# Kernel optimization log

Measured on AMD Instinct MI355X. Metric: run time of the kernel, lower is better.

## Reference

```python
import jax, jax.numpy as jnp
import numpy as np

B, N, C, H = 2, 4096, 256, 4
DH = C // H  # 64
EPS = 1e-6
TEMPERATURE = 1.0


def setup_inputs() -> dict:
    key = jax.random.key(0)
    ks = jax.random.split(key, 12)
    s = 0.02
    return {
        "x": jax.random.normal(ks[0], (B, N, C), dtype=jnp.float32),
        "pos_embed": jax.random.normal(ks[1], (B, N, C), dtype=jnp.float32),
        # per-head Q/K/V linear weights stacked over heads (torch Linear(dim, dim_head))
        "Wq": jax.random.normal(ks[2], (H, C, DH), dtype=jnp.float32) * s,
        "bq": jax.random.normal(ks[3], (H, DH), dtype=jnp.float32) * s,
        "Wk": jax.random.normal(ks[4], (H, C, DH), dtype=jnp.float32) * s,
        "bk": jax.random.normal(ks[5], (H, DH), dtype=jnp.float32) * s,
        "Wv": jax.random.normal(ks[6], (H, C, DH), dtype=jnp.float32) * s,
        "bv": jax.random.normal(ks[7], (H, DH), dtype=jnp.float32) * s,
        "Wo": jax.random.normal(ks[8], (C, C), dtype=jnp.float32) * s,
        "bo": jax.random.normal(ks[9], (C,), dtype=jnp.float32) * s,
        "ln_g": jnp.ones((C,), dtype=jnp.float32),
        "ln_b": jnp.zeros((C,), dtype=jnp.float32),
    }


def reference(x, pos_embed, Wq, bq, Wk, bk, Wv, bv, Wo, bo, ln_g, ln_b):
    dk = TEMPERATURE * jnp.sqrt(jnp.float32(DH))
    # pre-norm: x + pos_embed -> dropout(p=0, identity) -> LayerNorm(eps=1e-6)
    h = x + pos_embed
    mu = jnp.mean(h, axis=-1, keepdims=True)
    var = jnp.mean(jnp.square(h - mu), axis=-1, keepdims=True)
    h = (h - mu) * jax.lax.rsqrt(var + EPS) * ln_g + ln_b  # [B,N,C]
    # all heads at once (original loops over heads with separate small Linears)
    q = jnp.einsum("bnc,hcd->bhnd", h, Wq) + bq[None, :, None, :]
    k = jnp.einsum("bnc,hcd->bhnd", h, Wk) + bk[None, :, None, :]
    v = jnp.einsum("bnc,hcd->bhnd", h, Wv) + bv[None, :, None, :]
    scores = jnp.einsum("bhid,bhjd->bhij", q, k) / dk  # [B,H,N,N]
    # NOTE: original uses F.softmax(dot_prod, dim=1) on [B,N,N] -> normalize over
    # the QUERY axis i, not the key axis j. Replicated faithfully here (axis=2).
    attn = jax.nn.softmax(scores, axis=2)
    o = jnp.einsum("bhij,bhjd->bhid", attn, v)  # [B,H,N,DH]
    o = jnp.transpose(o, (0, 2, 1, 3)).reshape(B, N, C)  # concat heads on channel
    return o @ Wo + bo
```

## Files before the change

kernel.cpp:

```cpp
#include <hip/hip_runtime.h>
#include <math.h>

#define B_ 2
#define N_ 4096
#define C_ 256
#define H_ 4
#define DH_ 64
#define EPS_ 1e-6f
#define SCALE_Q_ 0.18033688011112042f

typedef short bf16x8 __attribute__((ext_vector_type(8)));
typedef short bf16x4v __attribute__((ext_vector_type(4)));
typedef float f32x4 __attribute__((ext_vector_type(4)));
typedef int i32x4 __attribute__((ext_vector_type(4)));

#define MFMA32(a, b, c) __builtin_amdgcn_mfma_f32_16x16x32_bf16(a, b, c, 0, 0, 0)
#define FAST_EXP2(x) __builtin_amdgcn_exp2f(x)

typedef const unsigned int __attribute__((address_space(1)))* gptr_as1;
typedef unsigned int __attribute__((address_space(3)))* lptr_as3;
#define GLL16(gp, lp)                                                   \
  __builtin_amdgcn_global_load_lds(                                     \
      (gptr_as1)(unsigned long long)(const void*)(gp),                  \
      (lptr_as3)(unsigned int)(unsigned long long)(const void*)(lp),    \
      16, 0, 0)

__device__ __forceinline__ unsigned short f2bf(float x) {
  unsigned int u = __float_as_uint(x);
  return (unsigned short)((u + 0x7FFFu + ((u >> 16) & 1u)) >> 16);
}
__device__ __forceinline__ float bf2f(unsigned short u) {
  return __uint_as_float(((unsigned int)u) << 16);
}
__device__ __forceinline__ int pack2bf(float lo, float hi) {
  return (int)__builtin_amdgcn_perm(__float_as_uint(hi) + 0x8000u,
                                    __float_as_uint(lo) + 0x8000u, 0x07060302u);
}

__global__ __launch_bounds__(256) void ln_kernel(
    const float* __restrict__ x, const float* __restrict__ pos,
    const float* __restrict__ g, const float* __restrict__ beta,
    unsigned short* __restrict__ h16) {
  const int w = threadIdx.x >> 6, lane = threadIdx.x & 63;
  const int row = blockIdx.x * 4 + w;
  const float4 xv = *(const float4*)&x[row * C_ + lane * 4];
  const float4 pv = *(const float4*)&pos[row * C_ + lane * 4];
  float4 v = {xv.x + pv.x, xv.y + pv.y, xv.z + pv.z, xv.w + pv.w};
  float s = v.x + v.y + v.z + v.w;
  s += __shfl_xor(s, 1);  s += __shfl_xor(s, 2);  s += __shfl_xor(s, 4);
  s += __shfl_xor(s, 8);  s += __shfl_xor(s, 16); s += __shfl_xor(s, 32);
  const float mu = s * (1.0f / C_);
  float4 d = {v.x - mu, v.y - mu, v.z - mu, v.w - mu};
  float q = d.x * d.x + d.y * d.y + d.z * d.z + d.w * d.w;
  q += __shfl_xor(q, 1);  q += __shfl_xor(q, 2);  q += __shfl_xor(q, 4);
  q += __shfl_xor(q, 8);  q += __shfl_xor(q, 16); q += __shfl_xor(q, 32);
  const float rs = rsqrtf(q * (1.0f / C_) + EPS_);
  const float4 g4 = *(const float4*)&g[lane * 4];
  const float4 b4 = *(const float4*)&beta[lane * 4];
  bf16x4v o;
  o[0] = (short)f2bf(d.x * rs * g4.x + b4.x);
  o[1] = (short)f2bf(d.y * rs * g4.y + b4.y);
  o[2] = (short)f2bf(d.z * rs * g4.z + b4.z);
  o[3] = (short)f2bf(d.w * rs * g4.w + b4.w);
  *(bf16x4v*)&h16[row * C_ + lane * 4] = o;
}

__global__ __launch_bounds__(256) void wconv_kernel(
    const float* __restrict__ Wq, const float* __restrict__ Wk,
    const float* __restrict__ Wv, const float* __restrict__ Wo,
    unsigned short* __restrict__ W3T, unsigned short* __restrict__ WoT) {
  const int base = blockIdx.x * 2048;
#pragma unroll
  for (int p = 0; p < 8; p++) {
    const int idx = base + p * 256 + threadIdx.x;
    if (idx < 196608) {
      const int m = idx >> 14;
      const int rem = idx & 16383;
      const int c = rem >> 6, d = rem & 63;
      const int h = m / 3, kind = m - h * 3;
      const float* W = kind == 0 ? Wq : kind == 1 ? Wk : Wv;
      float v = W[h * 16384 + rem];
      if (kind == 0) v *= SCALE_Q_;
      W3T[(h * 192 + kind * 64 + d) * 256 + c] = f2bf(v);
    } else {
      const int widx = idx - 196608;
      const int k = widx >> 8, n = widx & 255;
      WoT[n * 256 + k] = f2bf(Wo[widx]);
    }
  }
}

__global__ __launch_bounds__(256) void qkv_kernel(
    const unsigned short* __restrict__ h16, const unsigned short* __restrict__ W3T,
    const float* __restrict__ bq, const float* __restrict__ bk,
    const float* __restrict__ bv,
    unsigned short* __restrict__ q16, unsigned short* __restrict__ k16,
    unsigned short* __restrict__ vT16) {
  const int rt = blockIdx.x;
  const int hh = blockIdx.y;
  const int t = threadIdx.x;
  const int w = t >> 6, lane = t & 63, c = lane & 15, quad = lane >> 4;
  __shared__ unsigned short Hs[64 * 64];
  __shared__ unsigned short Bs[192 * 64];
  const int row0 = rt * 64;

  f32x4 acc[12];
#pragma unroll
  for (int nt = 0; nt < 12; nt++) acc[nt] = (f32x4){0.f, 0.f, 0.f, 0.f};

  for (int kt = 0; kt < C_; kt += 64) {
    __syncthreads();
#pragma unroll
    for (int p = 0; p < 2; p++) {
      const int e = t + p * 256;
      const int row = e >> 3, ch = e & 7;
      *(bf16x8*)&Hs[row * 64 + ((ch ^ (row & 7)) * 8)] =
          *(const bf16x8*)&h16[(size_t)(row0 + row) * C_ + kt + ch * 8];
    }
#pragma unroll
    for (int p = 0; p < 6; p++) {
      const int e = t + p * 256;
      const int row = e >> 3, ch = e & 7;
      *(bf16x8*)&Bs[row * 64 + ((ch ^ (row & 7)) * 8)] =
          *(const bf16x8*)&W3T[(size_t)(hh * 192 + row) * C_ + kt + ch * 8];
    }
    __syncthreads();
#pragma unroll
    for (int kh = 0; kh < 2; kh++) {
      const int i = w * 16 + c;
      bf16x8 a = *(const bf16x8*)&Hs[i * 64 + (((kh * 4 + quad) ^ (i & 7)) * 8)];
#pragma unroll
      for (int nt = 0; nt < 12; nt++) {
        const int n = nt * 16 + c;
        bf16x8 b = *(const bf16x8*)&Bs[n * 64 + (((kh * 4 + quad) ^ (n & 7)) * 8)];
        acc[nt] = MFMA32(a, b, acc[nt]);
      }
    }
  }
#pragma unroll
  for (int nt = 0; nt < 12; nt++) {
    const int kind = nt >> 2;
    const int col = (nt & 3) * 16 + c;
    const float bias = kind == 0 ? bq[hh * 64 + col] * SCALE_Q_
                     : kind == 1 ? bk[hh * 64 + col] : bv[hh * 64 + col];
#pragma unroll
    for (int r = 0; r < 4; r++) {
      const int gr = row0 + w * 16 + quad * 4 + r;
      const int b = gr >> 12, n = gr & (N_ - 1);
      const size_t bh = (size_t)(b * H_ + hh);
      const unsigned short val = f2bf(acc[nt][r] + bias);
      if (kind == 0)      q16[(bh * N_ + n) * DH_ + col] = val;
      else if (kind == 1) k16[(bh * N_ + n) * DH_ + col] = val;
      else                vT16[(bh * DH_ + col) * N_ + n] = val;
    }
  }
}

__global__ __launch_bounds__(256, 2) void colstats_kernel(
    const unsigned short* __restrict__ q16, const unsigned short* __restrict__ k16,
    unsigned short* __restrict__ vT16) {
  const int blk = blockIdx.x;
  const int bh = blk & 7;
  const int j0 = (blk >> 3) * 64;
  const int t = threadIdx.x;
  const int w = t >> 6, lane = t & 63, c = lane & 15, quad = lane >> 4;
  __shared__ __align__(16) unsigned short Qb[2 * 8192];
  __shared__ float Lp[4][64];
  __shared__ float ilv[64];

  bf16x8 ka[4][2];
#pragma unroll
  for (int jb = 0; jb < 4; jb++) {
    const size_t kb = ((size_t)bh * N_ + j0 + jb * 16 + c) * DH_;
    ka[jb][0] = *(const bf16x8*)&k16[kb + quad * 8];
    ka[jb][1] = *(const bf16x8*)&k16[kb + 32 + quad * 8];
  }

  const int rl = lane >> 3, sl = lane & 7;
  const unsigned short* gQ =
      q16 + ((size_t)bh * N_ + w * 32 + rl) * DH_ + ((sl ^ rl) * 8);
  const int woff = w * 2048;

  f32x4 lsum[4];
#pragma unroll
  for (int jb = 0; jb < 4; jb++) lsum[jb] = (f32x4){0.f, 0.f, 0.f, 0.f};

#pragma unroll
  for (int s = 0; s < 4; s++)
    GLL16(gQ + s * (8 * DH_), Qb + woff + s * 512);
  gQ += 128 * DH_;

  for (int r2 = 0; r2 < 32; r2 += 2) {
#pragma unroll
    for (int hf = 0; hf < 2; hf++) {
      const int cur = hf, nxt = hf ^ 1;
#pragma unroll
      for (int s = 0; s < 4; s++)
        GLL16(gQ + s * (8 * DH_), Qb + nxt * 8192 + woff + s * 512);
      gQ += 128 * DH_;
      asm volatile("s_waitcnt vmcnt(4)" ::: "memory");
      const unsigned short* Qs = Qb + cur * 8192 + woff;
#pragma unroll
      for (int u = 0; u < 2; u++) {
        bf16x8 qf0 = *(const bf16x8*)&Qs[u * 1024 + c * 64 + ((quad ^ (c & 7)) * 8)];
        bf16x8 qf1 = *(const bf16x8*)&Qs[u * 1024 + c * 64 + (((4 + quad) ^ (c & 7)) * 8)];
#pragma unroll
        for (int jb = 0; jb < 4; jb++) {
          f32x4 s = {0.f, 0.f, 0.f, 0.f};
          s = MFMA32(ka[jb][0], qf0, s);
          s = MFMA32(ka[jb][1], qf1, s);
#pragma unroll
          for (int r = 0; r < 4; r++) lsum[jb][r] += FAST_EXP2(s[r]);
        }
      }
    }
  }
#pragma unroll
  for (int jb = 0; jb < 4; jb++) {
#pragma unroll
    for (int r = 0; r < 4; r++) {
      float s = lsum[jb][r];
      s += __shfl_xor(s, 1); s += __shfl_xor(s, 2);
      s += __shfl_xor(s, 4); s += __shfl_xor(s, 8);
      if (c == 0) Lp[w][jb * 16 + quad * 4 + r] = s;
    }
  }
  __syncthreads();
  if (t < 64)
    ilv[t] = 1.0f / (Lp[0][t] + Lp[1][t] + Lp[2][t] + Lp[3][t]);
  __syncthreads();
  {
    const int d = t >> 2, chb = t & 3;
#pragma unroll
    for (int cc = 0; cc < 2; cc++) {
      const int ch = chb + cc * 4;
      const size_t addr = ((size_t)bh * DH_ + d) * N_ + j0 + ch * 8;
      bf16x8 v = *(const bf16x8*)&vT16[addr];
#pragma unroll
      for (int jj = 0; jj < 8; jj++)
        v[jj] = (short)f2bf(bf2f((unsigned short)v[jj]) * ilv[ch * 8 + jj]);
      *(bf16x8*)&vT16[addr] = v;
    }
  }
}

__global__ __launch_bounds__(512, 4) void attnout_kernel(
    const unsigned short* __restrict__ q16, const unsigned short* __restrict__ k16,
    const unsigned short* __restrict__ vT16, unsigned short* __restrict__ ob16) {
  const int blk = blockIdx.x;
  const int bh = blk & 7;
  const int bb = bh >> 2, hh = bh & 3;
  const int i0 = (blk >> 3) * 64;
  const int t = threadIdx.x;
  const int w = t >> 6, lane = t & 63, c = lane & 15, quad = lane >> 4;
  const int iw = w >> 2;
  const int jw = w & 3;

  __shared__ __align__(16) char smem[65536];
  unsigned short* S16 = (unsigned short*)smem;
  float* Rf = (float*)smem;

  bf16x8 qa[2][2];
#pragma unroll
  for (int ib = 0; ib < 2; ib++) {
    const size_t qb = ((size_t)bh * N_ + i0 + iw * 32 + ib * 16 + c) * DH_;
    qa[ib][0] = *(const bf16x8*)&q16[qb + quad * 8];
    qa[ib][1] = *(const bf16x8*)&q16[qb + 32 + quad * 8];
  }

  const int krow  = w * 16 + (lane >> 3);
  const int kch   = (lane & 7) ^ (((krow >> 2) & 7) ^ (krow & 3));
  const int krow2 = krow + 8;
  const int kch2  = (lane & 7) ^ (((krow2 >> 2) & 7) ^ (krow2 & 3));
  const unsigned short* gK  = k16 + ((size_t)bh * N_ + krow ) * DH_ + kch  * 8;
  const unsigned short* gK2 = k16 + ((size_t)bh * N_ + krow2) * DH_ + kch2 * 8;
  const int vd   = w * 8 + (lane >> 4);
  const int vch  = (lane & 15) ^ (vd & 15);
  const int vd2  = vd + 4;
  const int vch2 = (lane & 15) ^ (vd2 & 15);
  const unsigned short* gV  = vT16 + ((size_t)bh * DH_ + vd ) * N_ + vch  * 8;
  const unsigned short* gV2 = vT16 + ((size_t)bh * DH_ + vd2) * N_ + vch2 * 8;
  const int ldsKo = w * 1024;
  const int ldsVo = 8192 + w * 1024;

  f32x4 of[2][4];
#pragma unroll
  for (int ib = 0; ib < 2; ib++)
#pragma unroll
    for (int dt = 0; dt < 4; dt++) of[ib][dt] = (f32x4){0.f, 0.f, 0.f, 0.f};

  GLL16(gK,  S16 + ldsKo);       GLL16(gK2, S16 + ldsKo + 512);
  GLL16(gV,  S16 + ldsVo);       GLL16(gV2, S16 + ldsVo + 512);
  gK += 128 * DH_; gK2 += 128 * DH_; gV += 128; gV2 += 128;

  for (int jt = 0; jt < N_; jt += 256) {
#pragma unroll
    for (int half = 0; half < 2; half++) {
      const int cur = half, nxt = half ^ 1;
      GLL16(gK,  S16 + nxt * 16384 + ldsKo);
      GLL16(gK2, S16 + nxt * 16384 + ldsKo + 512);
      GLL16(gV,  S16 + nxt * 16384 + ldsVo);
      GLL16(gV2, S16 + nxt * 16384 + ldsVo + 512);
      gK += 128 * DH_; gK2 += 128 * DH_; gV += 128; gV2 += 128;
      asm volatile("s_waitcnt vmcnt(4)" ::: "memory");
      asm volatile("s_barrier" ::: "memory");
      const unsigned short* Ks = S16 + cur * 16384;
      const unsigned short* Vs = S16 + cur * 16384 + 8192;

      bf16x8 kf[2][2];
#pragma unroll
      for (int s = 0; s < 2; s++) {
        const int jr = jw * 32 + ((c >> 2) * 8) + s * 4 + (c & 3);
        const int swz = ((jr >> 2) & 7) ^ (jr & 3);
        kf[s][0] = *(const bf16x8*)&Ks[jr * 64 + ((quad ^ swz) * 8)];
        kf[s][1] = *(const bf16x8*)&Ks[jr * 64 + (((4 + quad) ^ swz) * 8)];
      }
      bf16x8 vf[4];
#pragma unroll
      for (int dt = 0; dt < 4; dt++) {
        const int d = dt * 16 + c;
        vf[dt] = *(const bf16x8*)&Vs[d * 128 + (((jw * 4 + quad) ^ (d & 15)) * 8)];
      }

      __builtin_amdgcn_s_setprio(1);
#pragma unroll
      for (int ib = 0; ib < 2; ib++) {
        f32x4 s0 = {0.f, 0.f, 0.f, 0.f}, s1 = {0.f, 0.f, 0.f, 0.f};
        s0 = MFMA32(kf[0][0], qa[ib][0], s0);
        s0 = MFMA32(kf[0][1], qa[ib][1], s0);
        s1 = MFMA32(kf[1][0], qa[ib][0], s1);
        s1 = MFMA32(kf[1][1], qa[ib][1], s1);
        i32x4 pi;
        pi[0] = pack2bf(FAST_EXP2(s0[0]), FAST_EXP2(s0[1]));
        pi[1] = pack2bf(FAST_EXP2(s0[2]), FAST_EXP2(s0[3]));
        pi[2] = pack2bf(FAST_EXP2(s1[0]), FAST_EXP2(s1[1]));
        pi[3] = pack2bf(FAST_EXP2(s1[2]), FAST_EXP2(s1[3]));
        bf16x8 pf = *(bf16x8*)&pi;
#pragma unroll
        for (int dt = 0; dt < 4; dt++)
          of[ib][dt] = MFMA32(pf, vf[dt], of[ib][dt]);
      }
      __builtin_amdgcn_s_setprio(0);
      asm volatile("s_barrier" ::: "memory");
    }
  }

  __syncthreads();
  if (jw >= 2) {
    float* dst = Rf + (iw * 2 + (jw - 2)) * 2048;
#pragma unroll
    for (int ib = 0; ib < 2; ib++)
#pragma unroll
      for (int dt = 0; dt < 4; dt++)
        *(f32x4*)&dst[lane * 32 + (((ib * 4 + dt) ^ (lane & 7)) * 4)] = of[ib][dt];
  }
  __syncthreads();
  if (jw < 2) {
    const float* src = Rf + (iw * 2 + jw) * 2048;
#pragma unroll
    for (int ib = 0; ib < 2; ib++)
#pragma unroll
      for (int dt = 0; dt < 4; dt++)
        of[ib][dt] += *(const f32x4*)&src[lane * 32 + (((ib * 4 + dt) ^ (lane & 7)) * 4)];
  }
  __syncthreads();
  if (jw == 1) {
    float* dst = Rf + iw * 2048;
#pragma unroll
    for (int ib = 0; ib < 2; ib++)
#pragma unroll
      for (int dt = 0; dt < 4; dt++)
        *(f32x4*)&dst[lane * 32 + (((ib * 4 + dt) ^ (lane & 7)) * 4)] = of[ib][dt];
  }
  __syncthreads();
  if (jw == 0) {
    const float* src = Rf + iw * 2048;
#pragma unroll
    for (int ib = 0; ib < 2; ib++)
#pragma unroll
      for (int dt = 0; dt < 4; dt++) {
        of[ib][dt] += *(const f32x4*)&src[lane * 32 + (((ib * 4 + dt) ^ (lane & 7)) * 4)];
#pragma unroll
        for (int r = 0; r < 4; r++)
          ob16[((size_t)bb * N_ + i0 + iw * 32 + ib * 16 + quad * 4 + r) * C_ +
               hh * DH_ + dt * 16 + c] = f2bf(of[ib][dt][r]);
      }
  }
}

__global__ __launch_bounds__(256) void outproj_kernel(
    const unsigned short* __restrict__ ob16, const unsigned short* __restrict__ WoT,
    const float* __restrict__ bo, float* __restrict__ out) {
  const int rt = blockIdx.x;
  const int ch2 = blockIdx.y;
  const int t = threadIdx.x;
  const int w = t >> 6, lane = t & 63, c = lane & 15, quad = lane >> 4;
  __shared__ unsigned short As[32 * 64];
  __shared__ unsigned short Bs[128 * 64];

  f32x4 acc[2][2];
#pragma unroll
  for (int mt = 0; mt < 2; mt++)
#pragma unroll
    for (int nt = 0; nt < 2; nt++) acc[mt][nt] = (f32x4){0.f, 0.f, 0.f, 0.f};

  for (int kt = 0; kt < C_; kt += 64) {
    __syncthreads();
    {
      const int row = t >> 3, ch = t & 7;
      *(bf16x8*)&As[row * 64 + ((ch ^ (row & 7)) * 8)] =
          *(const bf16x8*)&ob16[((size_t)rt * 32 + row) * C_ + kt + ch * 8];
    }
#pragma unroll
    for (int p = 0; p < 4; p++) {
      const int e = t + p * 256;
      const int row = e >> 3, ch = e & 7;
      *(bf16x8*)&Bs[row * 64 + ((ch ^ (row & 7)) * 8)] =
          *(const bf16x8*)&WoT[(size_t)(ch2 * 128 + row) * C_ + kt + ch * 8];
    }
    __syncthreads();
#pragma unroll
    for (int kh = 0; kh < 2; kh++) {
      bf16x8 a[2];
#pragma unroll
      for (int mt = 0; mt < 2; mt++) {
        const int i = mt * 16 + c;
        a[mt] = *(const bf16x8*)&As[i * 64 + (((kh * 4 + quad) ^ (i & 7)) * 8)];
      }
#pragma unroll
      for (int nt = 0; nt < 2; nt++) {
        const int n = w * 32 + nt * 16 + c;
        bf16x8 b = *(const bf16x8*)&Bs[n * 64 + (((kh * 4 + quad) ^ (n & 7)) * 8)];
        acc[0][nt] = MFMA32(a[0], b, acc[0][nt]);
        acc[1][nt] = MFMA32(a[1], b, acc[1][nt]);
      }
    }
  }
#pragma unroll
  for (int mt = 0; mt < 2; mt++)
#pragma unroll
    for (int nt = 0; nt < 2; nt++) {
      const int col = ch2 * 128 + w * 32 + nt * 16 + c;
      const float bias = bo[col];
#pragma unroll
      for (int r = 0; r < 4; r++)
        out[((size_t)rt * 32 + mt * 16 + quad * 4 + r) * C_ + col] = acc[mt][nt][r] + bias;
    }
}

extern "C" void kernel_launch(void* const* d_in, const int* in_sizes, int n_in,
                              void* d_out, int out_size, void* d_ws, size_t ws_size,
                              hipStream_t stream) {
  const float* x    = (const float*)d_in[0];
  const float* pos  = (const float*)d_in[1];
  const float* Wq   = (const float*)d_in[2];
  const float* bq   = (const float*)d_in[3];
  const float* Wk   = (const float*)d_in[4];
  const float* bk   = (const float*)d_in[5];
  const float* Wv   = (const float*)d_in[6];
  const float* bv   = (const float*)d_in[7];
  const float* Wo   = (const float*)d_in[8];
  const float* bo   = (const float*)d_in[9];
  const float* ln_g = (const float*)d_in[10];
  const float* ln_b = (const float*)d_in[11];
  float* out = (float*)d_out;

  const size_t SZ = (size_t)B_ * N_ * C_;
  unsigned short* h16  = (unsigned short*)d_ws;
  unsigned short* q16  = h16 + SZ;
  unsigned short* k16  = q16 + SZ;
  unsigned short* vT16 = k16 + SZ;
  unsigned short* ob16 = vT16 + SZ;
  unsigned short* W3T  = ob16 + SZ;
  unsigned short* WoT  = W3T + (size_t)H_ * 192 * 256;

  ln_kernel<<<B_ * N_ / 4, 256, 0, stream>>>(x, pos, ln_g, ln_b, h16);
  wconv_kernel<<<128, 256, 0, stream>>>(Wq, Wk, Wv, Wo, W3T, WoT);
  qkv_kernel<<<dim3(128, H_), 256, 0, stream>>>(h16, W3T, bq, bk, bv, q16, k16, vT16);
  colstats_kernel<<<512, 256, 0, stream>>>(q16, k16, vT16);
  attnout_kernel<<<512, 512, 0, stream>>>(q16, k16, vT16, ob16);
  outproj_kernel<<<dim3(256, 2), 256, 0, stream>>>(ob16, WoT, bo, out);
}
```

Measured before the change: 171.3 us.

## Halve attnout block to 4 waves, each covering all 64 query rows

Each attention-output block now runs 4 waves instead of 8. Every wave processes all 64 query rows (4 row-tiles) against its own slice of keys, where before two wave groups each took 32 rows. Each K/V fragment read from LDS now feeds twice as many MFMAs, and each wave issues more global-to-LDS loads. The cost is higher register pressure (more Q and accumulator fragments), fewer waves per block to hide latency, and a lower launch-bounds occupancy hint.

```diff
diff --git a/kernel.cpp b/kernel.cpp
--- a/kernel.cpp
+++ b/kernel.cpp
@@ -244,7 +244,7 @@
   }
 }
 
-__global__ __launch_bounds__(512, 4) void attnout_kernel(
+__global__ __launch_bounds__(256, 2) void attnout_kernel(
     const unsigned short* __restrict__ q16, const unsigned short* __restrict__ k16,
     const unsigned short* __restrict__ vT16, unsigned short* __restrict__ ob16) {
   const int blk = blockIdx.x;
@@ -253,56 +253,60 @@
   const int i0 = (blk >> 3) * 64;
   const int t = threadIdx.x;
   const int w = t >> 6, lane = t & 63, c = lane & 15, quad = lane >> 4;
-  const int iw = w >> 2;
-  const int jw = w & 3;
+  const int jw = w;
 
   __shared__ __align__(16) char smem[65536];
   unsigned short* S16 = (unsigned short*)smem;
   float* Rf = (float*)smem;
 
-  bf16x8 qa[2][2];
-#pragma unroll
-  for (int ib = 0; ib < 2; ib++) {
-    const size_t qb = ((size_t)bh * N_ + i0 + iw * 32 + ib * 16 + c) * DH_;
+  bf16x8 qa[4][2];
+#pragma unroll
+  for (int ib = 0; ib < 4; ib++) {
+    const size_t qb = ((size_t)bh * N_ + i0 + ib * 16 + c) * DH_;
     qa[ib][0] = *(const bf16x8*)&q16[qb + quad * 8];
     qa[ib][1] = *(const bf16x8*)&q16[qb + 32 + quad * 8];
   }
 
-  const int krow  = w * 16 + (lane >> 3);
-  const int kch   = (lane & 7) ^ (((krow >> 2) & 7) ^ (krow & 3));
-  const int krow2 = krow + 8;
-  const int kch2  = (lane & 7) ^ (((krow2 >> 2) & 7) ^ (krow2 & 3));
-  const unsigned short* gK  = k16 + ((size_t)bh * N_ + krow ) * DH_ + kch  * 8;
-  const unsigned short* gK2 = k16 + ((size_t)bh * N_ + krow2) * DH_ + kch2 * 8;
-  const int vd   = w * 8 + (lane >> 4);
-  const int vch  = (lane & 15) ^ (vd & 15);
-  const int vd2  = vd + 4;
-  const int vch2 = (lane & 15) ^ (vd2 & 15);
-  const unsigned short* gV  = vT16 + ((size_t)bh * DH_ + vd ) * N_ + vch  * 8;
-  const unsigned short* gV2 = vT16 + ((size_t)bh * DH_ + vd2) * N_ + vch2 * 8;
-  const int ldsKo = w * 1024;
-  const int ldsVo = 8192 + w * 1024;
-
-  f32x4 of[2][4];
-#pragma unroll
-  for (int ib = 0; ib < 2; ib++)
+  const int rl3 = lane >> 3, sl3 = lane & 7;
+  const int rl4 = lane >> 4, sl4 = lane & 15;
+  const unsigned short* gK[4];
+  const unsigned short* gV[4];
+#pragma unroll
+  for (int s = 0; s < 4; s++) {
+    const int kr = w * 32 + s * 8 + rl3;
+    const int kc = sl3 ^ (((kr >> 2) & 7) ^ (kr & 3));
+    gK[s] = k16 + ((size_t)bh * N_ + kr) * DH_ + kc * 8;
+    const int vd = w * 16 + s * 4 + rl4;
+    const int vc = sl4 ^ (vd & 15);
+    gV[s] = vT16 + ((size_t)bh * DH_ + vd) * N_ + vc * 8;
+  }
+  const int ldsKo = w * 2048;
+  const int ldsVo = 8192 + w * 2048;
+
+  f32x4 of[4][4];
+#pragma unroll
+  for (int ib = 0; ib < 4; ib++)
 #pragma unroll
     for (int dt = 0; dt < 4; dt++) of[ib][dt] = (f32x4){0.f, 0.f, 0.f, 0.f};
 
-  GLL16(gK,  S16 + ldsKo);       GLL16(gK2, S16 + ldsKo + 512);
-  GLL16(gV,  S16 + ldsVo);       GLL16(gV2, S16 + ldsVo + 512);
-  gK += 128 * DH_; gK2 += 128 * DH_; gV += 128; gV2 += 128;
+#pragma unroll
+  for (int s = 0; s < 4; s++) {
+    GLL16(gK[s], S16 + ldsKo + s * 512);
+    GLL16(gV[s], S16 + ldsVo + s * 512);
+    gK[s] += 128 * DH_; gV[s] += 128;
+  }
 
   for (int jt = 0; jt < N_; jt += 256) {
 #pragma unroll
     for (int half = 0; half < 2; half++) {
       const int cur = half, nxt = half ^ 1;
-      GLL16(gK,  S16 + nxt * 16384 + ldsKo);
-      GLL16(gK2, S16 + nxt * 16384 + ldsKo + 512);
-      GLL16(gV,  S16 + nxt * 16384 + ldsVo);
-      GLL16(gV2, S16 + nxt * 16384 + ldsVo + 512);
-      gK += 128 * DH_; gK2 += 128 * DH_; gV += 128; gV2 += 128;
-      asm volatile("s_waitcnt vmcnt(4)" ::: "memory");
+#pragma unroll
+      for (int s = 0; s < 4; s++) {
+        GLL16(gK[s], S16 + nxt * 16384 + ldsKo + s * 512);
+        GLL16(gV[s], S16 + nxt * 16384 + ldsVo + s * 512);
+        gK[s] += 128 * DH_; gV[s] += 128;
+      }
+      asm volatile("s_waitcnt vmcnt(8)" ::: "memory");
       asm volatile("s_barrier" ::: "memory");
       const unsigned short* Ks = S16 + cur * 16384;
       const unsigned short* Vs = S16 + cur * 16384 + 8192;
@@ -324,7 +328,7 @@
 
       __builtin_amdgcn_s_setprio(1);
 #pragma unroll
-      for (int ib = 0; ib < 2; ib++) {
+      for (int ib = 0; ib < 4; ib++) {
         f32x4 s0 = {0.f, 0.f, 0.f, 0.f}, s1 = {0.f, 0.f, 0.f, 0.f};
         s0 = MFMA32(kf[0][0], qa[ib][0], s0);
         s0 = MFMA32(kf[0][1], qa[ib][1], s0);
@@ -347,42 +351,42 @@
 
   __syncthreads();
   if (jw >= 2) {
-    float* dst = Rf + (iw * 2 + (jw - 2)) * 2048;
-#pragma unroll
-    for (int ib = 0; ib < 2; ib++)
+    float* dst = Rf + (jw - 2) * 4096;
+#pragma unroll
+    for (int ib = 0; ib < 4; ib++)
 #pragma unroll
       for (int dt = 0; dt < 4; dt++)
-        *(f32x4*)&dst[lane * 32 + (((ib * 4 + dt) ^ (lane & 7)) * 4)] = of[ib][dt];
+        *(f32x4*)&dst[lane * 64 + (((ib * 4 + dt) ^ (lane & 7)) * 4)] = of[ib][dt];
   }
   __syncthreads();
   if (jw < 2) {
-    const float* src = Rf + (iw * 2 + jw) * 2048;
-#pragma unroll
-    for (int ib = 0; ib < 2; ib++)
+    const float* src = Rf + jw * 4096;
+#pragma unroll
+    for (int ib = 0; ib < 4; ib++)
 #pragma unroll
       for (int dt = 0; dt < 4; dt++)
-        of[ib][dt] += *(const f32x4*)&src[lane * 32 + (((ib * 4 + dt) ^ (lane & 7)) * 4)];
+        of[ib][dt] += *(const f32x4*)&src[lane * 64 + (((ib * 4 + dt) ^ (lane & 7)) * 4)];
   }
   __syncthreads();
   if (jw == 1) {
-    float* dst = Rf + iw * 2048;
-#pragma unroll
-    for (int ib = 0; ib < 2; ib++)
+    float* dst = Rf;
+#pragma unroll
+    for (int ib = 0; ib < 4; ib++)
 #pragma unroll
       for (int dt = 0; dt < 4; dt++)
-        *(f32x4*)&dst[lane * 32 + (((ib * 4 + dt) ^ (lane & 7)) * 4)] = of[ib][dt];
+        *(f32x4*)&dst[lane * 64 + (((ib * 4 + dt) ^ (lane & 7)) * 4)] = of[ib][dt];
   }
   __syncthreads();
   if (jw == 0) {
-    const float* src = Rf + iw * 2048;
-#pragma unroll
-    for (int ib = 0; ib < 2; ib++)
+    const float* src = Rf;
+#pragma unroll
+    for (int ib = 0; ib < 4; ib++)
 #pragma unroll
       for (int dt = 0; dt < 4; dt++) {
-        of[ib][dt] += *(const f32x4*)&src[lane * 32 + (((ib * 4 + dt) ^ (lane & 7)) * 4)];
+        of[ib][dt] += *(const f32x4*)&src[lane * 64 + (((ib * 4 + dt) ^ (lane & 7)) * 4)];
 #pragma unroll
         for (int r = 0; r < 4; r++)
-          ob16[((size_t)bb * N_ + i0 + iw * 32 + ib * 16 + quad * 4 + r) * C_ +
+          ob16[((size_t)bb * N_ + i0 + ib * 16 + quad * 4 + r) * C_ +
                hh * DH_ + dt * 16 + c] = f2bf(of[ib][dt][r]);
       }
   }
@@ -478,6 +482,6 @@
   wconv_kernel<<<128, 256, 0, stream>>>(Wq, Wk, Wv, Wo, W3T, WoT);
   qkv_kernel<<<dim3(128, H_), 256, 0, stream>>>(h16, W3T, bq, bk, bv, q16, k16, vT16);
   colstats_kernel<<<512, 256, 0, stream>>>(q16, k16, vT16);
-  attnout_kernel<<<512, 512, 0, stream>>>(q16, k16, vT16, ob16);
+  attnout_kernel<<<512, 256, 0, stream>>>(q16, k16, vT16, ob16);
   outproj_kernel<<<dim3(256, 2), 256, 0, stream>>>(ob16, WoT, bo, out);
 }
```

Measured after the change: 172.2 us. No clear change (+0.5%).

## Merge LN and weight-conversion kernels; double-buffer QKV GEMM with direct-to-LDS loads

Applied to the files above, without the earlier changes.

The LayerNorm and weight bf16 conversion/transposition kernels are merged into one launch that picks its role from the block index, saving one kernel launch. The QKV projection GEMM now loads tiles with global_load_lds straight into a double-buffered shared-memory area, using s_waitcnt vmcnt plus raw barriers, so the next k-tile loads while the current one computes. This raises shared memory per block to 64KB, which may cut occupancy. The last prefetch also reads past the row's end into adjacent workspace, which is harmless but unused.

```diff
diff --git a/kernel.cpp b/kernel.cpp
--- a/kernel.cpp
+++ b/kernel.cpp
@@ -37,55 +37,55 @@
                                     __float_as_uint(lo) + 0x8000u, 0x07060302u);
 }
 
-__global__ __launch_bounds__(256) void ln_kernel(
+__global__ __launch_bounds__(256) void lnw_kernel(
     const float* __restrict__ x, const float* __restrict__ pos,
     const float* __restrict__ g, const float* __restrict__ beta,
-    unsigned short* __restrict__ h16) {
-  const int w = threadIdx.x >> 6, lane = threadIdx.x & 63;
-  const int row = blockIdx.x * 4 + w;
-  const float4 xv = *(const float4*)&x[row * C_ + lane * 4];
-  const float4 pv = *(const float4*)&pos[row * C_ + lane * 4];
-  float4 v = {xv.x + pv.x, xv.y + pv.y, xv.z + pv.z, xv.w + pv.w};
-  float s = v.x + v.y + v.z + v.w;
-  s += __shfl_xor(s, 1);  s += __shfl_xor(s, 2);  s += __shfl_xor(s, 4);
-  s += __shfl_xor(s, 8);  s += __shfl_xor(s, 16); s += __shfl_xor(s, 32);
-  const float mu = s * (1.0f / C_);
-  float4 d = {v.x - mu, v.y - mu, v.z - mu, v.w - mu};
-  float q = d.x * d.x + d.y * d.y + d.z * d.z + d.w * d.w;
-  q += __shfl_xor(q, 1);  q += __shfl_xor(q, 2);  q += __shfl_xor(q, 4);
-  q += __shfl_xor(q, 8);  q += __shfl_xor(q, 16); q += __shfl_xor(q, 32);
-  const float rs = rsqrtf(q * (1.0f / C_) + EPS_);
-  const float4 g4 = *(const float4*)&g[lane * 4];
-  const float4 b4 = *(const float4*)&beta[lane * 4];
-  bf16x4v o;
-  o[0] = (short)f2bf(d.x * rs * g4.x + b4.x);
-  o[1] = (short)f2bf(d.y * rs * g4.y + b4.y);
-  o[2] = (short)f2bf(d.z * rs * g4.z + b4.z);
-  o[3] = (short)f2bf(d.w * rs * g4.w + b4.w);
-  *(bf16x4v*)&h16[row * C_ + lane * 4] = o;
-}
-
-__global__ __launch_bounds__(256) void wconv_kernel(
+    unsigned short* __restrict__ h16,
     const float* __restrict__ Wq, const float* __restrict__ Wk,
     const float* __restrict__ Wv, const float* __restrict__ Wo,
     unsigned short* __restrict__ W3T, unsigned short* __restrict__ WoT) {
-  const int base = blockIdx.x * 2048;
-#pragma unroll
-  for (int p = 0; p < 8; p++) {
-    const int idx = base + p * 256 + threadIdx.x;
-    if (idx < 196608) {
-      const int m = idx >> 14;
-      const int rem = idx & 16383;
-      const int c = rem >> 6, d = rem & 63;
-      const int h = m / 3, kind = m - h * 3;
-      const float* W = kind == 0 ? Wq : kind == 1 ? Wk : Wv;
-      float v = W[h * 16384 + rem];
-      if (kind == 0) v *= SCALE_Q_;
-      W3T[(h * 192 + kind * 64 + d) * 256 + c] = f2bf(v);
-    } else {
-      const int widx = idx - 196608;
-      const int k = widx >> 8, n = widx & 255;
-      WoT[n * 256 + k] = f2bf(Wo[widx]);
+  if (blockIdx.x < 2048) {
+    const int w = threadIdx.x >> 6, lane = threadIdx.x & 63;
+    const int row = blockIdx.x * 4 + w;
+    const float4 xv = *(const float4*)&x[row * C_ + lane * 4];
+    const float4 pv = *(const float4*)&pos[row * C_ + lane * 4];
+    float4 v = {xv.x + pv.x, xv.y + pv.y, xv.z + pv.z, xv.w + pv.w};
+    float s = v.x + v.y + v.z + v.w;
+    s += __shfl_xor(s, 1);  s += __shfl_xor(s, 2);  s += __shfl_xor(s, 4);
+    s += __shfl_xor(s, 8);  s += __shfl_xor(s, 16); s += __shfl_xor(s, 32);
+    const float mu = s * (1.0f / C_);
+    float4 d = {v.x - mu, v.y - mu, v.z - mu, v.w - mu};
+    float q = d.x * d.x + d.y * d.y + d.z * d.z + d.w * d.w;
+    q += __shfl_xor(q, 1);  q += __shfl_xor(q, 2);  q += __shfl_xor(q, 4);
+    q += __shfl_xor(q, 8);  q += __shfl_xor(q, 16); q += __shfl_xor(q, 32);
+    const float rs = rsqrtf(q * (1.0f / C_) + EPS_);
+    const float4 g4 = *(const float4*)&g[lane * 4];
+    const float4 b4 = *(const float4*)&beta[lane * 4];
+    bf16x4v o;
+    o[0] = (short)f2bf(d.x * rs * g4.x + b4.x);
+    o[1] = (short)f2bf(d.y * rs * g4.y + b4.y);
+    o[2] = (short)f2bf(d.z * rs * g4.z + b4.z);
+    o[3] = (short)f2bf(d.w * rs * g4.w + b4.w);
+    *(bf16x4v*)&h16[row * C_ + lane * 4] = o;
+  } else {
+    const int base = (blockIdx.x - 2048) * 2048;
+#pragma unroll
+    for (int p = 0; p < 8; p++) {
+      const int idx = base + p * 256 + threadIdx.x;
+      if (idx < 196608) {
+        const int m = idx >> 14;
+        const int rem = idx & 16383;
+        const int cc = rem >> 6, dd = rem & 63;
+        const int h = m / 3, kind = m - h * 3;
+        const float* W = kind == 0 ? Wq : kind == 1 ? Wk : Wv;
+        float v = W[h * 16384 + rem];
+        if (kind == 0) v *= SCALE_Q_;
+        W3T[(h * 192 + kind * 64 + dd) * 256 + cc] = f2bf(v);
+      } else {
+        const int widx = idx - 196608;
+        const int k = widx >> 8, n = widx & 255;
+        WoT[n * 256 + k] = f2bf(Wo[widx]);
+      }
     }
   }
 }
@@ -100,41 +100,63 @@
   const int hh = blockIdx.y;
   const int t = threadIdx.x;
   const int w = t >> 6, lane = t & 63, c = lane & 15, quad = lane >> 4;
-  __shared__ unsigned short Hs[64 * 64];
-  __shared__ unsigned short Bs[192 * 64];
+  __shared__ __align__(16) unsigned short S16[2 * 16384];
   const int row0 = rt * 64;
 
   f32x4 acc[12];
 #pragma unroll
   for (int nt = 0; nt < 12; nt++) acc[nt] = (f32x4){0.f, 0.f, 0.f, 0.f};
 
-  for (int kt = 0; kt < C_; kt += 64) {
-    __syncthreads();
-#pragma unroll
-    for (int p = 0; p < 2; p++) {
-      const int e = t + p * 256;
-      const int row = e >> 3, ch = e & 7;
-      *(bf16x8*)&Hs[row * 64 + ((ch ^ (row & 7)) * 8)] =
-          *(const bf16x8*)&h16[(size_t)(row0 + row) * C_ + kt + ch * 8];
-    }
-#pragma unroll
-    for (int p = 0; p < 6; p++) {
-      const int e = t + p * 256;
-      const int row = e >> 3, ch = e & 7;
-      *(bf16x8*)&Bs[row * 64 + ((ch ^ (row & 7)) * 8)] =
-          *(const bf16x8*)&W3T[(size_t)(hh * 192 + row) * C_ + kt + ch * 8];
-    }
-    __syncthreads();
-#pragma unroll
-    for (int kh = 0; kh < 2; kh++) {
-      const int i = w * 16 + c;
-      bf16x8 a = *(const bf16x8*)&Hs[i * 64 + (((kh * 4 + quad) ^ (i & 7)) * 8)];
-#pragma unroll
-      for (int nt = 0; nt < 12; nt++) {
-        const int n = nt * 16 + c;
-        bf16x8 b = *(const bf16x8*)&Bs[n * 64 + (((kh * 4 + quad) ^ (n & 7)) * 8)];
-        acc[nt] = MFMA32(a, b, acc[nt]);
-      }
+  const int rl = lane >> 3, sl = lane & 7;
+  const int chq = (sl ^ rl) * 8;
+  const unsigned short* gH[2];
+  const unsigned short* gB[6];
+#pragma unroll
+  for (int p = 0; p < 2; p++)
+    gH[p] = h16 + (size_t)(row0 + p * 32 + w * 8 + rl) * C_ + chq;
+#pragma unroll
+  for (int p = 0; p < 6; p++)
+    gB[p] = W3T + (size_t)(hh * 192 + p * 32 + w * 8 + rl) * C_ + chq;
+
+#pragma unroll
+  for (int p = 0; p < 2; p++) GLL16(gH[p], S16 + p * 2048 + w * 512);
+#pragma unroll
+  for (int p = 0; p < 6; p++) GLL16(gB[p], S16 + 4096 + p * 2048 + w * 512);
+#pragma unroll
+  for (int p = 0; p < 2; p++) gH[p] += 64;
+#pragma unroll
+  for (int p = 0; p < 6; p++) gB[p] += 64;
+
+  for (int kt2 = 0; kt2 < 2; kt2++) {
+#pragma unroll
+    for (int hf = 0; hf < 2; hf++) {
+      const int cur = hf, nxt = hf ^ 1;
+#pragma unroll
+      for (int p = 0; p < 2; p++)
+        GLL16(gH[p], S16 + nxt * 16384 + p * 2048 + w * 512);
+#pragma unroll
+      for (int p = 0; p < 6; p++)
+        GLL16(gB[p], S16 + nxt * 16384 + 4096 + p * 2048 + w * 512);
+#pragma unroll
+      for (int p = 0; p < 2; p++) gH[p] += 64;
+#pragma unroll
+      for (int p = 0; p < 6; p++) gB[p] += 64;
+      asm volatile("s_waitcnt vmcnt(8)" ::: "memory");
+      asm volatile("s_barrier" ::: "memory");
+      const unsigned short* Hs = S16 + cur * 16384;
+      const unsigned short* Bs = S16 + cur * 16384 + 4096;
+#pragma unroll
+      for (int kh = 0; kh < 2; kh++) {
+        const int i = w * 16 + c;
+        bf16x8 a = *(const bf16x8*)&Hs[i * 64 + (((kh * 4 + quad) ^ (i & 7)) * 8)];
+#pragma unroll
+        for (int nt = 0; nt < 12; nt++) {
+          const int n = nt * 16 + c;
+          bf16x8 b = *(const bf16x8*)&Bs[n * 64 + (((kh * 4 + quad) ^ (n & 7)) * 8)];
+          acc[nt] = MFMA32(a, b, acc[nt]);
+        }
+      }
+      asm volatile("s_barrier" ::: "memory");
     }
   }
 #pragma unroll
@@ -474,8 +496,8 @@
   unsigned short* W3T  = ob16 + SZ;
   unsigned short* WoT  = W3T + (size_t)H_ * 192 * 256;
 
-  ln_kernel<<<B_ * N_ / 4, 256, 0, stream>>>(x, pos, ln_g, ln_b, h16);
-  wconv_kernel<<<128, 256, 0, stream>>>(Wq, Wk, Wv, Wo, W3T, WoT);
+  lnw_kernel<<<2176, 256, 0, stream>>>(x, pos, ln_g, ln_b, h16,
+                                       Wq, Wk, Wv, Wo, W3T, WoT);
   qkv_kernel<<<dim3(128, H_), 256, 0, stream>>>(h16, W3T, bq, bk, bv, q16, k16, vT16);
   colstats_kernel<<<512, 256, 0, stream>>>(q16, k16, vT16);
   attnout_kernel<<<512, 512, 0, stream>>>(q16, k16, vT16, ob16);
```

Measured after the change: 175.6 us. 1.03x slower.
